# Kernel tuning notes

Hardware: AMD Instinct MI355X
Metric: run time of the kernel (lower is better)

Reference implementation:

```python
import jax, jax.numpy as jnp
import numpy as np

N = 16384
D_IN = 64
D_HID = D_IN // 2  # 32
D_OUT = 32


def setup_inputs() -> dict:
    key = jax.random.key(0)
    kA, kX, k1, k2, k3 = jax.random.split(key, 5)
    # Dense adjacency-like operator [N, N]; scaled so activations stay sane.
    A = jax.random.normal(kA, (N, N), dtype=jnp.float32) / np.sqrt(N)
    X = jax.random.normal(kX, (N, D_IN), dtype=jnp.float32)
    # torch nn.Linear weights: [out_features, in_features], no bias
    W1 = jax.random.normal(k1, (D_IN, D_IN), dtype=jnp.float32) / np.sqrt(D_IN)
    W2 = jax.random.normal(k2, (D_HID, D_IN), dtype=jnp.float32) / np.sqrt(D_IN)
    W3 = jax.random.normal(k3, (D_OUT, D_HID), dtype=jnp.float32) / np.sqrt(D_HID)
    return {"A": A, "X": X, "W1": W1, "W2": W2, "W3": W3}


def reference(A, X, W1, W2, W3):
    # Layer 1: relu(fc1(A @ X)); fc(x) = x @ W.T
    h = jax.nn.relu((A @ X) @ W1.T)        # [N, D_IN]
    # Layer 2: relu(fc2(A @ h))
    h = jax.nn.relu((A @ h) @ W2.T)        # [N, D_HID]
    # Layer 3: fc3(A @ h), no activation
    return (A @ h) @ W3.T                  # [N, D_OUT]
```

## Files before the change

kernel.cpp:

```cpp
#include <hip/hip_runtime.h>
#include <cstdint>
#include <cstddef>


#define NN 16384
#define SK1 8
#define KC1 (NN / SK1)
#define SK2 16
#define KC2 (NN / SK2)
#define NKB (NN / 32)

typedef __attribute__((ext_vector_type(8))) short s16x8;
typedef __attribute__((ext_vector_type(4))) float fx4;

__device__ __forceinline__ unsigned short f2bf_rne(float f) {
    unsigned int x = __builtin_bit_cast(unsigned int, f);
    x += 0x7fffu + ((x >> 16) & 1u);
    return (unsigned short)(x >> 16);
}

__device__ __forceinline__ s16x8 pack_bf(fx4 a, fx4 b) {
    s16x8 t;
    t[0] = (short)f2bf_rne(a[0]);
    t[1] = (short)f2bf_rne(a[1]);
    t[2] = (short)f2bf_rne(a[2]);
    t[3] = (short)f2bf_rne(a[3]);
    t[4] = (short)f2bf_rne(b[0]);
    t[5] = (short)f2bf_rne(b[1]);
    t[6] = (short)f2bf_rne(b[2]);
    t[7] = (short)f2bf_rne(b[3]);
    return t;
}

__global__ __launch_bounds__(256) void k_conv(
    const float* __restrict__ A32, unsigned short* __restrict__ Abf)
{
    const int lane = threadIdx.x & 63;
    const int wv   = threadIdx.x >> 6;
    const int srow = lane & 15, kg = lane >> 4;
    const long w = blockIdx.x * 4 + wv;
    const long u0 = w * 64;
#pragma unroll 4
    for (int j = 0; j < 64; ++j) {
        const long u = u0 + j;
        const long g = u >> 9;
        const long kblk = u & (NKB - 1);
        const float* p = A32 + (g * 16 + srow) * (long)NN + kblk * 32 + kg * 4;
        fx4 a0 = __builtin_nontemporal_load((const fx4*)p);
        fx4 a1 = __builtin_nontemporal_load((const fx4*)(p + 16));
        *(s16x8*)(Abf + (u * 64 + lane) * 8) = pack_bf(a0, a1);
    }
}

template <int ASRC>
__global__ __launch_bounds__(256, 4) void k_spmm1(
    const float* __restrict__ A32,
    const unsigned short* __restrict__ Abf,
    const unsigned short* __restrict__ PT,
    float* __restrict__ part)
{
    const int lane = threadIdx.x & 63;
    const int wv   = threadIdx.x >> 6;
    const int srow = lane & 15;
    const int kg   = lane >> 4;
    const int s    = blockIdx.y;
    const long kbeg = (long)s * KC1;
    const int rowbase = blockIdx.x * 128 + wv * 32;
    const long r0 = rowbase + srow;
    const long r1 = rowbase + 16 + srow;
    const long g0 = rowbase >> 4, g1 = g0 + 1;

    fx4 acc0[4], acc1[4];
#pragma unroll
    for (int c = 0; c < 4; ++c) {
        acc0[c] = (fx4){0.f, 0.f, 0.f, 0.f};
        acc1[c] = (fx4){0.f, 0.f, 0.f, 0.f};
    }

#pragma unroll 2
    for (int i = 0; i < KC1 / 32; ++i) {
        const long ko = kbeg + (long)i * 32;
        const long kblk = ko >> 5;
        s16x8 af0, af1;
        if (ASRC) {
            af0 = *(const s16x8*)(Abf + ((g0 * NKB + kblk) * 64 + lane) * 8);
            af1 = *(const s16x8*)(Abf + ((g1 * NKB + kblk) * 64 + lane) * 8);
        } else {
            const float* p0 = A32 + r0 * (long)NN + ko + kg * 4;
            const float* p1 = A32 + r1 * (long)NN + ko + kg * 4;
            fx4 a00 = __builtin_nontemporal_load((const fx4*)p0);
            fx4 a01 = __builtin_nontemporal_load((const fx4*)(p0 + 16));
            fx4 a10 = __builtin_nontemporal_load((const fx4*)p1);
            fx4 a11 = __builtin_nontemporal_load((const fx4*)(p1 + 16));
            af0 = pack_bf(a00, a01);
            af1 = pack_bf(a10, a11);
        }
#pragma unroll
        for (int c = 0; c < 4; ++c) {
            s16x8 bf = *(const s16x8*)(PT + (long)(c * 16 + srow) * NN + ko + kg * 8);
            acc0[c] = __builtin_amdgcn_mfma_f32_16x16x32_bf16(af0, bf, acc0[c], 0, 0, 0);
            acc1[c] = __builtin_amdgcn_mfma_f32_16x16x32_bf16(af1, bf, acc1[c], 0, 0, 0);
        }
    }
    float* pbase = part + (long)s * NN * 64;
#pragma unroll
    for (int c = 0; c < 4; ++c)
#pragma unroll
        for (int r = 0; r < 4; ++r) {
            pbase[(long)(rowbase + kg * 4 + r) * 64 + c * 16 + srow]      = acc0[c][r];
            pbase[(long)(rowbase + 16 + kg * 4 + r) * 64 + c * 16 + srow] = acc1[c][r];
        }
}

template <int ABF>
__global__ __launch_bounds__(256, 4) void k_spmm2(
    const unsigned short* __restrict__ Abf,
    const float* __restrict__ A32,
    const unsigned short* __restrict__ PT,
    float* __restrict__ part)
{
    const int lane = threadIdx.x & 63;
    const int wv   = threadIdx.x >> 6;
    const int srow = lane & 15;
    const int kg   = lane >> 4;
    const int s    = blockIdx.y;
    const long kbeg = (long)s * KC2;
    const int rowbase = blockIdx.x * 256 + wv * 64;
    const long g0 = rowbase >> 4;

    fx4 acc[4][2];
#pragma unroll
    for (int t = 0; t < 4; ++t)
#pragma unroll
        for (int c = 0; c < 2; ++c) acc[t][c] = (fx4){0.f, 0.f, 0.f, 0.f};

#pragma unroll 2
    for (int i = 0; i < KC2 / 32; ++i) {
        const long ko = kbeg + (long)i * 32;
        const long kblk = ko >> 5;
        s16x8 af[4];
        if (ABF) {
#pragma unroll
            for (int t = 0; t < 4; ++t)
                af[t] = *(const s16x8*)(Abf + (((g0 + t) * NKB + kblk) * 64 + lane) * 8);
        } else {
#pragma unroll
            for (int t = 0; t < 4; ++t) {
                const float* p = A32 + (long)(rowbase + t * 16 + srow) * NN + ko + kg * 4;
                fx4 a0 = __builtin_nontemporal_load((const fx4*)p);
                fx4 a1 = __builtin_nontemporal_load((const fx4*)(p + 16));
                af[t] = pack_bf(a0, a1);
            }
        }
        s16x8 b0 = *(const s16x8*)(PT + (long)srow * NN + ko + kg * 8);
        s16x8 b1 = *(const s16x8*)(PT + (long)(16 + srow) * NN + ko + kg * 8);
#pragma unroll
        for (int t = 0; t < 4; ++t) {
            acc[t][0] = __builtin_amdgcn_mfma_f32_16x16x32_bf16(af[t], b0, acc[t][0], 0, 0, 0);
            acc[t][1] = __builtin_amdgcn_mfma_f32_16x16x32_bf16(af[t], b1, acc[t][1], 0, 0, 0);
        }
    }
    float* pbase = part + (long)s * NN * 32;
#pragma unroll
    for (int t = 0; t < 4; ++t)
#pragma unroll
        for (int c = 0; c < 2; ++c)
#pragma unroll
            for (int r = 0; r < 4; ++r)
                pbase[(long)(rowbase + t * 16 + kg * 4 + r) * 32 + c * 16 + srow] = acc[t][c][r];
}

template <int DIN, int DOUT, int NSUM, bool RELU>
__global__ __launch_bounds__(256) void k_proj(
    const float* __restrict__ src,
    const float* __restrict__ W,
    unsigned short* __restrict__ PT)
{
    __shared__ float Ws[DOUT * DIN];
    __shared__ float Hs[64][DIN + 1];
    const int tid = threadIdx.x;
    for (int i = tid; i < DOUT * DIN; i += 256) Ws[i] = W[i];
    const int rbase = blockIdx.x * 64;
    for (int i = tid; i < 64 * DIN; i += 256) {
        const int rl = i / DIN, k = i % DIN;
        float v = 0.f;
#pragma unroll
        for (int s2 = 0; s2 < NSUM; ++s2)
            v += src[(long)s2 * NN * DIN + (long)(rbase + rl) * DIN + k];
        Hs[rl][k] = RELU ? fmaxf(v, 0.f) : v;
    }
    __syncthreads();
    const int rl = tid & 63;
    const int c0 = tid >> 6;
    const int r  = rbase + rl;
    const int kk = r & 31;
    const int pidx = (r & ~31) + ((kk & 15) >> 2) * 8 + (kk & 3) + ((kk >> 4) << 2);
    for (int c = c0; c < DOUT; c += 4) {
        float accv = 0.f;
#pragma unroll
        for (int k = 0; k < DIN; ++k) accv += Hs[rl][k] * Ws[c * DIN + k];
        PT[(long)c * NN + pidx] = f2bf_rne(accv);
    }
}

__global__ __launch_bounds__(256) void k_red(
    const float* __restrict__ part, float* __restrict__ out)
{
    const int e = blockIdx.x * 256 + threadIdx.x;
    if (e >= NN * 32 / 4) return;
    fx4 v = (fx4){0.f, 0.f, 0.f, 0.f};
#pragma unroll
    for (int s = 0; s < SK2; ++s)
        v += *(const fx4*)(part + (long)s * NN * 32 + (long)e * 4);
    *(fx4*)(out + (long)e * 4) = v;
}

extern "C" void kernel_launch(void* const* d_in, const int* in_sizes, int n_in,
                              void* d_out, int out_size, void* d_ws, size_t ws_size,
                              hipStream_t stream) {
    const float* A  = (const float*)d_in[0];
    const float* X  = (const float*)d_in[1];
    const float* W1 = (const float*)d_in[2];
    const float* W2 = (const float*)d_in[3];
    const float* W3 = (const float*)d_in[4];
    float* out = (float*)d_out;

    char* ws = (char*)d_ws;
    const size_t part_b = (size_t)SK1 * NN * 64 * 4;
    const size_t pt_b   = (size_t)64 * NN * 2;
    const size_t abf_b  = (size_t)NN * NN * 2;
    float*          part = (float*)ws;
    unsigned short* PT   = (unsigned short*)(ws + part_b);
    unsigned short* Abf  = (unsigned short*)(ws + part_b + pt_b);
    const bool save = ws_size >= part_b + pt_b + abf_b;

    dim3 b(256);
    dim3 gP(NN / 64);
    dim3 g1(NN / 128, SK1);
    dim3 g2(NN / 256, SK2);

    k_proj<64, 64, 1, false><<<gP, b, 0, stream>>>(X, W1, PT);
    if (save) {
        k_conv<<<dim3(2048), b, 0, stream>>>(A, Abf);
        k_spmm1<1><<<g1, b, 0, stream>>>(A, Abf, PT, part);
    } else {
        k_spmm1<0><<<g1, b, 0, stream>>>(A, Abf, PT, part);
    }

    k_proj<64, 32, SK1, true><<<gP, b, 0, stream>>>(part, W2, PT);
    if (save) k_spmm2<1><<<g2, b, 0, stream>>>(Abf, A, PT, part);
    else      k_spmm2<0><<<g2, b, 0, stream>>>(Abf, A, PT, part);

    k_proj<32, 32, SK2, true><<<gP, b, 0, stream>>>(part, W3, PT);
    if (save) k_spmm2<1><<<g2, b, 0, stream>>>(Abf, A, PT, part);
    else      k_spmm2<0><<<g2, b, 0, stream>>>(Abf, A, PT, part);

    k_red<<<dim3(NN * 32 / 4 / 256), b, 0, stream>>>(part, out);
}
```

Baseline: 754.4 us.

## Stage fp32-to-bf16 conversion of A through swizzled LDS for coalesced row reads

The A conversion kernel now uses 1024-thread blocks that each own 16 rows. Every wave streams contiguous 512-float chunks of one row into a double-buffered, XOR-swizzled LDS tile, then re-reads the tile in the MFMA fragment layout and writes the packed bf16 output. Previously each lane read 16-byte pieces scattered across 16 rows. The goal is fully coalesced global reads of the 1 GB fp32 matrix. In exchange it adds 64 KB of LDS per block, which limits occupancy, plus a barrier per chunk.

```diff
diff --git a/kernel.cpp b/kernel.cpp
--- a/kernel.cpp
+++ b/kernel.cpp
@@ -9,6 +9,8 @@
 #define SK2 16
 #define KC2 (NN / SK2)
 #define NKB (NN / 32)
+#define CVK 512
+#define CVNC (NN / CVK)
 
 typedef __attribute__((ext_vector_type(8))) short s16x8;
 typedef __attribute__((ext_vector_type(4))) float fx4;
@@ -32,23 +34,42 @@
     return t;
 }
 
-__global__ __launch_bounds__(256) void k_conv(
+__global__ __launch_bounds__(1024) void k_conv(
     const float* __restrict__ A32, unsigned short* __restrict__ Abf)
 {
-    const int lane = threadIdx.x & 63;
-    const int wv   = threadIdx.x >> 6;
+    __shared__ float Asm[2][16][CVK];
+    const int tid = threadIdx.x;
+    const int w = tid >> 6, lane = tid & 63;
     const int srow = lane & 15, kg = lane >> 4;
-    const long w = blockIdx.x * 4 + wv;
-    const long u0 = w * 64;
-#pragma unroll 4
-    for (int j = 0; j < 64; ++j) {
-        const long u = u0 + j;
-        const long g = u >> 9;
-        const long kblk = u & (NKB - 1);
-        const float* p = A32 + (g * 16 + srow) * (long)NN + kblk * 32 + kg * 4;
-        fx4 a0 = __builtin_nontemporal_load((const fx4*)p);
-        fx4 a1 = __builtin_nontemporal_load((const fx4*)(p + 16));
-        *(s16x8*)(Abf + (u * 64 + lane) * 8) = pack_bf(a0, a1);
+    const long g = blockIdx.x;
+    const float* arow = A32 + (g * 16 + w) * (long)NN;
+    fx4 ld0, ld1;
+
+    auto LOAD = [&](int c) {
+        ld0 = __builtin_nontemporal_load((const fx4*)(arow + (long)c * CVK + lane * 4));
+        ld1 = __builtin_nontemporal_load((const fx4*)(arow + (long)c * CVK + 256 + lane * 4));
+    };
+    auto LDSW = [&](int buf) {
+        const int sw = (w & 7) << 2;
+        *(fx4*)&Asm[buf][w][(lane * 4) ^ sw]       = ld0;
+        *(fx4*)&Asm[buf][w][(256 + lane * 4) ^ sw] = ld1;
+    };
+    auto EMIT = [&](int buf, int c) {
+        const int base = w * 32 + kg * 4;
+        const int sw = (srow & 7) << 2;
+        fx4 a0 = *(const fx4*)&Asm[buf][srow][base ^ sw];
+        fx4 a1 = *(const fx4*)&Asm[buf][srow][(base + 16) ^ sw];
+        *(s16x8*)(Abf + ((g * NKB + (long)(c * 16 + w)) * 64 + lane) * 8) = pack_bf(a0, a1);
+    };
+
+    LOAD(0);
+    LDSW(0);
+    __syncthreads();
+    for (int c = 0; c < CVNC; ++c) {
+        if (c + 1 < CVNC) LOAD(c + 1);
+        EMIT(c & 1, c);
+        if (c + 1 < CVNC) LDSW((c + 1) & 1);
+        __syncthreads();
     }
 }
 
@@ -241,7 +262,7 @@
 
     k_proj<64, 64, 1, false><<<gP, b, 0, stream>>>(X, W1, PT);
     if (save) {
-        k_conv<<<dim3(2048), b, 0, stream>>>(A, Abf);
+        k_conv<<<dim3(NN / 16), dim3(1024), 0, stream>>>(A, Abf);
         k_spmm1<1><<<g1, b, 0, stream>>>(A, Abf, PT, part);
     } else {
         k_spmm1<0><<<g1, b, 0, stream>>>(A, Abf, PT, part);
```

Result: faster. 727.8 us (-3.5%).
